# Kernel tuning notes

Measured on AMD Instinct MI355X. Metric: run time of the kernel, lower is better.

## Reference

```python
import jax, jax.numpy as jnp
import numpy as np

TOPK = 8
EPS = 1e-12  # F.normalize eps


def setup_inputs() -> dict:
    key = jax.random.key(0)
    k1, k2 = jax.random.split(key)
    feats = jax.random.normal(k1, (4, 256, 64, 64), dtype=jnp.float32)
    logits = jax.random.normal(k2, (4, 1, 64, 64), dtype=jnp.float32)
    return {"feats": feats, "logits": logits}


def reference(feats, logits):
    b, c, h, w = feats.shape
    n = h * w
    feat_flat = feats.reshape(b, c, n)
    # F.normalize(dim=1): x / max(||x||_2, eps)
    norm = jnp.sqrt(jnp.sum(feat_flat * feat_flat, axis=1, keepdims=True))
    feat_norm = feat_flat / jnp.maximum(norm, EPS)
    # sim[b,i,j] = <f_i, f_j>  -> [B, N, N]
    sim = jnp.einsum('bci,bcj->bij', feat_norm, feat_norm)
    k = min(TOPK, n)
    _, idx = jax.lax.top_k(sim, k)  # [B, N, k] indices
    prob = jax.nn.sigmoid(logits).reshape(b, n)  # [B, N]
    # gathered[b,i,j] = prob[b, idx[b,i,j]]
    gathered = jax.vmap(lambda p, i: p[i])(prob, idx)  # [B, N, k]
    anchor = prob[:, :, None]  # [B, N, 1] broadcast over k
    loss = jnp.mean(jnp.abs(anchor - gathered))
    return loss
```

## Files before the change

### kernel.cpp

```cpp
#include <hip/hip_runtime.h>
#include <hip/hip_bf16.h>

typedef _Float16 half8 __attribute__((ext_vector_type(8)));
typedef unsigned short ushort8 __attribute__((ext_vector_type(8)));
typedef float floatx4 __attribute__((ext_vector_type(4)));

#define B_ 4
#define C_ 256
#define N_ 4096
#define NT 32
#define TRI 528

#define OFF_FN    ((size_t)0)
#define OFF_PROB  ((size_t)(8u << 20))
#define OFF_PART  (OFF_PROB + 65536)
#define OFF_TOP   ((size_t)(16u << 20))

__device__ __forceinline__ void gl_lds16(const void* g, void* l) {
    __builtin_amdgcn_global_load_lds(
        (const __attribute__((address_space(1))) void*)g,
        (__attribute__((address_space(3))) void*)l,
        16, 0, 0);
}

__device__ __forceinline__ void cas(uint32_t& a, uint32_t& b) {
    uint32_t hi = max(a, b); b = min(a, b); a = hi;
}

__device__ __forceinline__ void sort8(uint32_t v[8]) {
    cas(v[0],v[1]); cas(v[2],v[3]); cas(v[4],v[5]); cas(v[6],v[7]);
    cas(v[0],v[2]); cas(v[1],v[3]); cas(v[4],v[6]); cas(v[5],v[7]);
    cas(v[1],v[2]); cas(v[5],v[6]);
    cas(v[0],v[4]); cas(v[1],v[5]); cas(v[2],v[6]); cas(v[3],v[7]);
    cas(v[2],v[4]); cas(v[3],v[5]);
    cas(v[1],v[2]); cas(v[3],v[4]); cas(v[5],v[6]);
}

__device__ __forceinline__ void merge8(uint32_t r[8], const uint32_t n[8]) {
    uint32_t m[8];
#pragma unroll
    for (int i = 0; i < 8; ++i) m[i] = max(r[i], n[7 - i]);
    cas(m[0],m[4]); cas(m[1],m[5]); cas(m[2],m[6]); cas(m[3],m[7]);
    cas(m[0],m[2]); cas(m[1],m[3]); cas(m[4],m[6]); cas(m[5],m[7]);
    cas(m[0],m[1]); cas(m[2],m[3]); cas(m[4],m[5]); cas(m[6],m[7]);
#pragma unroll
    for (int i = 0; i < 8; ++i) r[i] = m[i];
}

#define TS 68
__global__ __launch_bounds__(256) void prep_kernel(const float* __restrict__ feats,
                                                   const float* __restrict__ logits,
                                                   _Float16* __restrict__ fn,
                                                   float* __restrict__ prob) {
    __shared__ __align__(16) float T[C_ * TS];
    __shared__ float S[256];
    __shared__ float I[64];

    const int t  = threadIdx.x;
    const int b  = blockIdx.x >> 6;
    const int i0 = (blockIdx.x & 63) * 64;
    const float* fb = feats + (size_t)b * C_ * N_;

#pragma unroll
    for (int k = 0; k < 16; ++k) {
        int ch = t + k * 256;
        int row = ch >> 4, col4 = ch & 15;
        float4 v = *(const float4*)(fb + (size_t)row * N_ + i0 + col4 * 4);
        *(float4*)&T[row * TS + col4 * 4] = v;
    }
    __syncthreads();
    {
        int i = t & 63, cq = t >> 6;
        float ss = 0.f;
#pragma unroll 8
        for (int j = 0; j < 64; ++j) { float v = T[(cq * 64 + j) * TS + i]; ss += v * v; }
        S[cq * 64 + i] = ss;
    }
    __syncthreads();
    if (t < 64) {
        float ss = S[t] + S[64 + t] + S[128 + t] + S[192 + t];
        I[t] = 1.f / fmaxf(sqrtf(ss), 1e-12f);
        float lg = logits[b * N_ + i0 + t];
        prob[b * N_ + i0 + t] = 1.f / (1.f + expf(-lg));
    }
    __syncthreads();
    {
        int i = t >> 2, chunk = t & 3;
        float s = I[i];
        _Float16* fr = fn + ((size_t)(b * N_ + i0 + i)) * C_ + chunk * 64;
#pragma unroll
        for (int v8 = 0; v8 < 8; ++v8) {
            half8 h;
#pragma unroll
            for (int e = 0; e < 8; ++e)
                h[e] = (_Float16)(T[(chunk * 64 + v8 * 8 + e) * TS + i] * s);
            *(half8*)(fr + v8 * 8) = h;
        }
    }
}

#define CSH 136
__global__ __launch_bounds__(256, 4) void gram_sel_kernel(const _Float16* __restrict__ fn,
                                                          uint32_t* __restrict__ top) {
    __shared__ __align__(16) char smem[128 * CSH * 2];
    _Float16* As = (_Float16*)smem;
    _Float16* Bs = (_Float16*)(smem + 16384);
    unsigned short* Ch = (unsigned short*)smem;
    uint32_t* Ms = (uint32_t*)smem;

    const int t    = threadIdx.x;
    const int lane = t & 63;
    const int w    = t >> 6;
    const int m16  = lane & 15;
    const int q    = lane >> 4;

    const int bid0 = blockIdx.x;
    const int bid  = (bid0 & 7) * 264 + (bid0 >> 3);

    const int b = bid / TRI;
    const int u = bid - b * TRI;
    int it = (int)(32.5f - sqrtf(32.5f * 32.5f - 2.0f * (float)u));
    while (u >= (it + 1) * (65 - (it + 1)) / 2) ++it;
    while (u < it * (65 - it) / 2) --it;
    const int jt = it + (u - it * (65 - it) / 2);
    const bool diag = (it == jt);

    const int i0 = it * 128, j0 = jt * 128;
    const _Float16* fnb = fn + (size_t)b * N_ * C_;

    const int srowb = t >> 3;
    const int schunk = (t & 7) ^ (srowb & 7);
    const int sw = m16 & 7;

    floatx4 acc[2][8];
#pragma unroll
    for (int ri = 0; ri < 2; ++ri)
#pragma unroll
        for (int jj = 0; jj < 8; ++jj) acc[ri][jj] = floatx4{0.f, 0.f, 0.f, 0.f};

    for (int kc = 0; kc < 4; ++kc) {
#pragma unroll
        for (int r = 0; r < 4; ++r) {
            int row = r * 32 + srowb;
            const _Float16* gA = fnb + (size_t)(i0 + row) * C_ + kc * 64 + schunk * 8;
            const _Float16* gB = fnb + (size_t)(j0 + row) * C_ + kc * 64 + schunk * 8;
            gl_lds16(gA, (char*)As + r * 4096 + t * 16);
            gl_lds16(gB, (char*)Bs + r * 4096 + t * 16);
        }
        __syncthreads();
#pragma unroll
        for (int kk = 0; kk < 2; ++kk) {
            half8 a0 = *(const half8*)&As[(w * 32 + m16) * 64 + ((kk * 4 + q) ^ sw) * 8];
            half8 a1 = *(const half8*)&As[(w * 32 + 16 + m16) * 64 + ((kk * 4 + q) ^ sw) * 8];
#pragma unroll
            for (int jj = 0; jj < 8; ++jj) {
                half8 bf = *(const half8*)&Bs[(jj * 16 + m16) * 64 + ((kk * 4 + q) ^ sw) * 8];
                acc[0][jj] = __builtin_amdgcn_mfma_f32_16x16x32_f16(a0, bf, acc[0][jj], 0, 0, 0);
                acc[1][jj] = __builtin_amdgcn_mfma_f32_16x16x32_f16(a1, bf, acc[1][jj], 0, 0, 0);
            }
        }
        __syncthreads();
    }

#pragma unroll
    for (int jj = 0; jj < 8; ++jj)
#pragma unroll
        for (int ri = 0; ri < 2; ++ri) {
            const int col = jj * 16 + m16;
            const int row = w * 32 + ri * 16 + q * 4;
#pragma unroll
            for (int p = 0; p < 2; ++p) {
                auto pk2 = __builtin_amdgcn_cvt_pkrtz(acc[ri][jj][2 * p], acc[ri][jj][2 * p + 1]);
                uint32_t bits = __builtin_bit_cast(uint32_t, pk2);
                uint32_t s = (bits >> 15) & 0x00010001u;
                uint32_t fl = bits ^ (s * 0x7FFFu + 0x80008000u);
                *(uint32_t*)&Ch[col * CSH + row + 2 * p] = fl;
            }
        }
    __syncthreads();

    uint32_t cpk[8], rpk[8];
    {
        const int ccol = t >> 1, cr0 = (t & 1) * 64;
        const unsigned short* cc = &Ch[ccol * CSH + cr0];
        const int ibase = i0 + cr0;
#pragma unroll
        for (int g = 0; g < 8; ++g) {
            ushort8 v = *(const ushort8*)(cc + g * 8);
            uint32_t cand[8];
#pragma unroll
            for (int e = 0; e < 8; ++e)
                cand[e] = ((uint32_t)v[e] << 16) | (uint32_t)(ibase + g * 8 + e);
            sort8(cand);
            if (g == 0) {
#pragma unroll
                for (int s = 0; s < 8; ++s) cpk[s] = cand[s];
            } else merge8(cpk, cand);
        }
    }
    if (!diag) {
        const int rrow = t >> 1, ch0 = (t & 1) * 64;
        const unsigned short* cr = &Ch[ch0 * CSH + rrow];
        const int jbase = j0 + ch0;
#pragma unroll
        for (int g = 0; g < 8; ++g) {
            uint32_t cand[8];
#pragma unroll
            for (int e = 0; e < 8; ++e)
                cand[e] = ((uint32_t)cr[(g * 8 + e) * CSH] << 16) | (uint32_t)(jbase + g * 8 + e);
            sort8(cand);
            if (g == 0) {
#pragma unroll
                for (int s = 0; s < 8; ++s) rpk[s] = cand[s];
            } else merge8(rpk, cand);
        }
    }
    __syncthreads();

    if (t & 1) {
#pragma unroll
        for (int s = 0; s < 8; ++s) Ms[(t >> 1) * 8 + s] = cpk[s];
        if (!diag) {
#pragma unroll
            for (int s = 0; s < 8; ++s) Ms[1024 + (t >> 1) * 8 + s] = rpk[s];
        }
    }
    __syncthreads();
    if (!(t & 1)) {
        uint32_t o[8];
#pragma unroll
        for (int s = 0; s < 8; ++s) o[s] = Ms[(t >> 1) * 8 + s];
        merge8(cpk, o);
        uint32_t* dst = top + (((size_t)b * N_ + j0 + (t >> 1)) * 32 + it) * 8;
        *(uint4*)dst       = make_uint4(cpk[0], cpk[1], cpk[2], cpk[3]);
        *(uint4*)(dst + 4) = make_uint4(cpk[4], cpk[5], cpk[6], cpk[7]);
        if (!diag) {
#pragma unroll
            for (int s = 0; s < 8; ++s) o[s] = Ms[1024 + (t >> 1) * 8 + s];
            merge8(rpk, o);
            uint32_t* dst2 = top + (((size_t)b * N_ + i0 + (t >> 1)) * 32 + jt) * 8;
            *(uint4*)dst2       = make_uint4(rpk[0], rpk[1], rpk[2], rpk[3]);
            *(uint4*)(dst2 + 4) = make_uint4(rpk[4], rpk[5], rpk[6], rpk[7]);
        }
    }
}

__global__ __launch_bounds__(256) void merge_kernel(const uint32_t* __restrict__ top,
                                                    const float* __restrict__ prob,
                                                    float* __restrict__ partials) {
    __shared__ float red[4];
    const int t = threadIdx.x;
    const int lane = t & 63;
    const int w = t >> 6;
    const int rg = blockIdx.x * 4 + w;
    const int b = rg >> 12;

    uint4 v4 = ((const uint4*)(top + (size_t)rg * 256))[lane];
    uint32_t v[4] = {v4.x, v4.y, v4.z, v4.w};
    uint32_t m = max(max(v[0], v[1]), max(v[2], v[3]));

    const float* pb = prob + (b << 12);
    float p_r = prob[rg];
    float contrib = 0.f;
#pragma unroll
    for (int k = 0; k < 8; ++k) {
        uint32_t M = m;
#pragma unroll
        for (int off = 32; off; off >>= 1) M = max(M, (uint32_t)__shfl_xor((int)M, off));
        if (lane == k) contrib = fabsf(p_r - pb[M & 0xFFFu]);
#pragma unroll
        for (int s = 0; s < 4; ++s) v[s] = (v[s] == M) ? 0u : v[s];
        m = max(max(v[0], v[1]), max(v[2], v[3]));
    }
#pragma unroll
    for (int off = 32; off; off >>= 1) contrib += __shfl_xor(contrib, off);
    if (lane == 0) red[w] = contrib;
    __syncthreads();
    if (t == 0) partials[blockIdx.x] = red[0] + red[1] + red[2] + red[3];
}

__global__ __launch_bounds__(256) void final_kernel(const float* __restrict__ partials,
                                                    float* __restrict__ out) {
    __shared__ float red[256];
    int t = threadIdx.x;
    float s = 0.f;
#pragma unroll
    for (int k = 0; k < 16; ++k) s += partials[k * 256 + t];
    red[t] = s;
    __syncthreads();
    for (int off = 128; off > 0; off >>= 1) {
        if (t < off) red[t] += red[t + off];
        __syncthreads();
    }
    if (t == 0) out[0] = red[0] * (1.f / (B_ * N_ * 8.0f));
}

extern "C" void kernel_launch(void* const* d_in, const int* in_sizes, int n_in,
                              void* d_out, int out_size, void* d_ws, size_t ws_size,
                              hipStream_t stream) {
    const float* feats  = (const float*)d_in[0];
    const float* logits = (const float*)d_in[1];
    float* out = (float*)d_out;
    char* ws = (char*)d_ws;
    _Float16* fn   = (_Float16*)(ws + OFF_FN);
    float* prob    = (float*)(ws + OFF_PROB);
    float* parts   = (float*)(ws + OFF_PART);
    uint32_t* top  = (uint32_t*)(ws + OFF_TOP);

    prep_kernel<<<256, 256, 0, stream>>>(feats, logits, fn, prob);
    gram_sel_kernel<<<B_ * TRI, 256, 0, stream>>>(fn, top);
    merge_kernel<<<4096, 256, 0, stream>>>(top, prob, parts);
    final_kernel<<<1, 256, 0, stream>>>(parts, out);
}
```

Measured before the change: 129.4 us.

## Split gram tile epilogue into two column halves to cut LDS and raise occupancy

The epilogue now stages the 128x128 similarity tile through shared memory in two 64-column halves instead of all at once. This shrinks the shared buffer from about 34.8KB to 32KB and raises the launch-bounds occupancy hint from 4 to 5 blocks per CU. Column top-8 selection now uses four threads per column with a 4-way merge, and row selection accumulates across both halves. The cost is extra barriers and more merge work per column, plus tighter register limits that may cause spills.

New measurement: 145.7 us. 1.13x slower.

```diff
diff --git a/kernel.cpp b/kernel.cpp
--- a/kernel.cpp
+++ b/kernel.cpp
@@ -100,13 +100,16 @@
 }
 
 #define CSH 136
-__global__ __launch_bounds__(256, 4) void gram_sel_kernel(const _Float16* __restrict__ fn,
+#define MSC_OFF 17408
+#define MSR_OFF 23552
+__global__ __launch_bounds__(256, 5) void gram_sel_kernel(const _Float16* __restrict__ fn,
                                                           uint32_t* __restrict__ top) {
-    __shared__ __align__(16) char smem[128 * CSH * 2];
+    __shared__ __align__(16) char smem[32768];
     _Float16* As = (_Float16*)smem;
     _Float16* Bs = (_Float16*)(smem + 16384);
     unsigned short* Ch = (unsigned short*)smem;
-    uint32_t* Ms = (uint32_t*)smem;
+    uint32_t* MsC = (uint32_t*)(smem + MSC_OFF);
+    uint32_t* MsR = (uint32_t*)(smem + MSR_OFF);
 
     const int t    = threadIdx.x;
     const int lane = t & 63;
@@ -162,81 +165,98 @@
         __syncthreads();
     }
 
-#pragma unroll
-    for (int jj = 0; jj < 8; ++jj)
-#pragma unroll
-        for (int ri = 0; ri < 2; ++ri) {
-            const int col = jj * 16 + m16;
-            const int row = w * 32 + ri * 16 + q * 4;
-#pragma unroll
-            for (int p = 0; p < 2; ++p) {
-                auto pk2 = __builtin_amdgcn_cvt_pkrtz(acc[ri][jj][2 * p], acc[ri][jj][2 * p + 1]);
-                uint32_t bits = __builtin_bit_cast(uint32_t, pk2);
-                uint32_t s = (bits >> 15) & 0x00010001u;
-                uint32_t fl = bits ^ (s * 0x7FFFu + 0x80008000u);
-                *(uint32_t*)&Ch[col * CSH + row + 2 * p] = fl;
-            }
-        }
-    __syncthreads();
-
-    uint32_t cpk[8], rpk[8];
-    {
-        const int ccol = t >> 1, cr0 = (t & 1) * 64;
-        const unsigned short* cc = &Ch[ccol * CSH + cr0];
-        const int ibase = i0 + cr0;
-#pragma unroll
-        for (int g = 0; g < 8; ++g) {
-            ushort8 v = *(const ushort8*)(cc + g * 8);
-            uint32_t cand[8];
-#pragma unroll
-            for (int e = 0; e < 8; ++e)
-                cand[e] = ((uint32_t)v[e] << 16) | (uint32_t)(ibase + g * 8 + e);
-            sort8(cand);
-            if (g == 0) {
-#pragma unroll
-                for (int s = 0; s < 8; ++s) cpk[s] = cand[s];
-            } else merge8(cpk, cand);
-        }
-    }
+    uint32_t rpk[8] = {0,0,0,0,0,0,0,0};
+
+#pragma unroll
+    for (int h = 0; h < 2; ++h) {
+        if (h) __syncthreads();
+
+#pragma unroll
+        for (int jh = 0; jh < 4; ++jh) {
+            const int jj = 4 * h + jh;
+#pragma unroll
+            for (int ri = 0; ri < 2; ++ri) {
+                const int col = jh * 16 + m16;
+                const int row = w * 32 + ri * 16 + q * 4;
+#pragma unroll
+                for (int p = 0; p < 2; ++p) {
+                    auto pk2 = __builtin_amdgcn_cvt_pkrtz(acc[ri][jj][2 * p], acc[ri][jj][2 * p + 1]);
+                    uint32_t bits = __builtin_bit_cast(uint32_t, pk2);
+                    uint32_t s = (bits >> 15) & 0x00010001u;
+                    uint32_t fl = bits ^ (s * 0x7FFFu + 0x80008000u);
+                    *(uint32_t*)&Ch[col * CSH + row + 2 * p] = fl;
+                }
+            }
+        }
+        __syncthreads();
+
+        uint32_t cpk[8];
+        {
+            const int ccol = t >> 2, cr0 = (t & 3) * 32;
+            const unsigned short* cc = &Ch[ccol * CSH + cr0];
+            const int ibase = i0 + cr0;
+#pragma unroll
+            for (int g = 0; g < 4; ++g) {
+                ushort8 v = *(const ushort8*)(cc + g * 8);
+                uint32_t cand[8];
+#pragma unroll
+                for (int e = 0; e < 8; ++e)
+                    cand[e] = ((uint32_t)v[e] << 16) | (uint32_t)(ibase + g * 8 + e);
+                sort8(cand);
+                if (g == 0) {
+#pragma unroll
+                    for (int s = 0; s < 8; ++s) cpk[s] = cand[s];
+                } else merge8(cpk, cand);
+            }
+        }
+        if (!diag) {
+            const int rrow = t >> 1, c0 = (t & 1) * 32;
+            const unsigned short* cr = &Ch[c0 * CSH + rrow];
+            const int jbase = j0 + h * 64 + c0;
+#pragma unroll
+            for (int g = 0; g < 4; ++g) {
+                uint32_t cand[8];
+#pragma unroll
+                for (int e = 0; e < 8; ++e)
+                    cand[e] = ((uint32_t)cr[(g * 8 + e) * CSH] << 16) | (uint32_t)(jbase + g * 8 + e);
+                sort8(cand);
+                if (h == 0 && g == 0) {
+#pragma unroll
+                    for (int s = 0; s < 8; ++s) rpk[s] = cand[s];
+                } else merge8(rpk, cand);
+            }
+        }
+        if (t & 3) {
+#pragma unroll
+            for (int s = 0; s < 8; ++s)
+                MsC[(t >> 2) * 24 + ((t & 3) - 1) * 8 + s] = cpk[s];
+        }
+        __syncthreads();
+        if (!(t & 3)) {
+            uint32_t o[8];
+#pragma unroll
+            for (int m = 0; m < 3; ++m) {
+#pragma unroll
+                for (int s = 0; s < 8; ++s) o[s] = MsC[(t >> 2) * 24 + m * 8 + s];
+                merge8(cpk, o);
+            }
+            uint32_t* dst = top + (((size_t)b * N_ + j0 + h * 64 + (t >> 2)) * 32 + it) * 8;
+            *(uint4*)dst       = make_uint4(cpk[0], cpk[1], cpk[2], cpk[3]);
+            *(uint4*)(dst + 4) = make_uint4(cpk[4], cpk[5], cpk[6], cpk[7]);
+        }
+    }
+
     if (!diag) {
-        const int rrow = t >> 1, ch0 = (t & 1) * 64;
-        const unsigned short* cr = &Ch[ch0 * CSH + rrow];
-        const int jbase = j0 + ch0;
-#pragma unroll
-        for (int g = 0; g < 8; ++g) {
-            uint32_t cand[8];
-#pragma unroll
-            for (int e = 0; e < 8; ++e)
-                cand[e] = ((uint32_t)cr[(g * 8 + e) * CSH] << 16) | (uint32_t)(jbase + g * 8 + e);
-            sort8(cand);
-            if (g == 0) {
-#pragma unroll
-                for (int s = 0; s < 8; ++s) rpk[s] = cand[s];
-            } else merge8(rpk, cand);
-        }
-    }
-    __syncthreads();
-
-    if (t & 1) {
-#pragma unroll
-        for (int s = 0; s < 8; ++s) Ms[(t >> 1) * 8 + s] = cpk[s];
-        if (!diag) {
-#pragma unroll
-            for (int s = 0; s < 8; ++s) Ms[1024 + (t >> 1) * 8 + s] = rpk[s];
-        }
-    }
-    __syncthreads();
-    if (!(t & 1)) {
-        uint32_t o[8];
-#pragma unroll
-        for (int s = 0; s < 8; ++s) o[s] = Ms[(t >> 1) * 8 + s];
-        merge8(cpk, o);
-        uint32_t* dst = top + (((size_t)b * N_ + j0 + (t >> 1)) * 32 + it) * 8;
-        *(uint4*)dst       = make_uint4(cpk[0], cpk[1], cpk[2], cpk[3]);
-        *(uint4*)(dst + 4) = make_uint4(cpk[4], cpk[5], cpk[6], cpk[7]);
-        if (!diag) {
-#pragma unroll
-            for (int s = 0; s < 8; ++s) o[s] = Ms[1024 + (t >> 1) * 8 + s];
+        __syncthreads();
+        if (t & 1) {
+#pragma unroll
+            for (int s = 0; s < 8; ++s) MsR[(t >> 1) * 8 + s] = rpk[s];
+        }
+        __syncthreads();
+        if (!(t & 1)) {
+            uint32_t o[8];
+#pragma unroll
+            for (int s = 0; s < 8; ++s) o[s] = MsR[(t >> 1) * 8 + s];
             merge8(rpk, o);
             uint32_t* dst2 = top + (((size_t)b * N_ + i0 + (t >> 1)) * 32 + jt) * 8;
             *(uint4*)dst2       = make_uint4(rpk[0], rpk[1], rpk[2], rpk[3]);
```
